# Optimization experiments

Measured on AMD Instinct MI355X. Metric: run time of the kernel, lower is better.

The kernel has to match this reference:

```python
import jax, jax.numpy as jnp
import numpy as np

N = 50000      # nodes
E = 800000     # edges
IN = 128       # in_channels
H = 128        # hidden_channels
C = 40         # num_classes
L = 2          # num_layers
BN_EPS = 1e-5


def setup_inputs() -> dict:
    key = jax.random.key(0)
    ks = jax.random.split(key, 16)
    s = 0.02
    return {
        "x": jax.random.normal(ks[0], (N, IN), dtype=jnp.float32),
        "edge_index": jax.random.randint(ks[1], (2, E), 0, N, dtype=jnp.int64),
        "fc0_w": jax.random.normal(ks[2], (H, IN), dtype=jnp.float32) * s,
        "fc0_b": jnp.zeros((H,), dtype=jnp.float32),
        "conv_w": jax.random.normal(ks[3], (L, H, H), dtype=jnp.float32) * s,
        "W_w": jax.random.normal(ks[4], (H, H), dtype=jnp.float32) * s,
        "W_b": jnp.zeros((H,), dtype=jnp.float32),
        "bn_gamma": jnp.ones((L + 1, H), dtype=jnp.float32),
        "bn_beta": jnp.zeros((L + 1, H), dtype=jnp.float32),
        "fc_out_w": jax.random.normal(ks[5], (H, H), dtype=jnp.float32) * s,
        "fc_out_b": jnp.zeros((H,), dtype=jnp.float32),
        "out_w": jax.random.normal(ks[6], (C, H), dtype=jnp.float32) * s,
        "out_b": jnp.zeros((C,), dtype=jnp.float32),
    }


def _bn_eval(x, gamma, beta):
    # eval-mode BatchNorm1d with default running stats (mean=0, var=1)
    return x * (gamma / jnp.sqrt(1.0 + BN_EPS)) + beta


def _gcn_conv(x, w, src, dst, norm, n):
    # x' = D^{-1/2} (A + I) D^{-1/2} (x @ w^T), bias=False
    xw = x @ w.T                        # [N, H]
    msg = xw[src] * norm[:, None]       # [E+N, H] gather + scale
    return jax.ops.segment_sum(msg, dst, num_segments=n)


def reference(x, edge_index, fc0_w, fc0_b, conv_w, W_w, W_b, bn_gamma, bn_beta,
              fc_out_w, fc_out_b, out_w, out_b):
    n = x.shape[0]
    loops = jnp.arange(n, dtype=edge_index.dtype)
    src = jnp.concatenate([edge_index[0], loops])   # add self-loops
    dst = jnp.concatenate([edge_index[1], loops])
    deg = jax.ops.segment_sum(jnp.ones_like(dst, dtype=x.dtype), dst, num_segments=n)
    deg_isqrt = jax.lax.rsqrt(deg)                  # deg >= 1 (self-loops)
    norm = deg_isqrt[src] * deg_isqrt[dst]          # [E+N]

    h = x @ fc0_w.T + fc0_b
    h = _bn_eval(h, bn_gamma[0], bn_beta[0])
    h = jax.nn.relu(h)                              # dropout: eval mode -> identity

    jk = h
    for i in range(L):
        h = _gcn_conv(h, conv_w[i], src, dst, norm, n)
        h = h @ W_w.T + W_b
        h = _bn_eval(h, bn_gamma[i + 1], bn_beta[i + 1])
        h = jax.nn.relu(h)
        jk = jnp.maximum(jk, h)                     # JumpingKnowledge 'max'

    out = jk @ fc_out_w.T + fc_out_b
    return out @ out_w.T + out_b
```

## Files before the change

kernel.cpp:

```cpp
#include <hip/hip_runtime.h>

#define NN 50000
#define NE 800000
#define EN 850000
#define NB 196
#define BINBLK 391
#define CAPE 5120
#define CAPT 5376

static constexpr float BN_SC = 0.99999500003749968f;

typedef __bf16 bf16x8 __attribute__((ext_vector_type(8)));
typedef float  f32x4  __attribute__((ext_vector_type(4)));

__device__ __forceinline__ float4 ld4(const float* p){ return *reinterpret_cast<const float4*>(p); }

__device__ __forceinline__ unsigned short f2bf(float f){
  union { float f; unsigned int i; } v; v.f = f;
  unsigned int r = v.i + 0x7fffu + ((v.i >> 16) & 1u);
  return (unsigned short)(r >> 16);
}
__device__ __forceinline__ float lo2f(unsigned int u){
  union { unsigned int i; float f; } v; v.i = u << 16; return v.f;
}
__device__ __forceinline__ float hi2f(unsigned int u){
  union { unsigned int i; float f; } v; v.i = u & 0xffff0000u; return v.f;
}
__device__ __forceinline__ unsigned int pk2(float flo, float fhi){
  return (unsigned int)f2bf(flo) | ((unsigned int)f2bf(fhi) << 16);
}
__device__ __forceinline__ int fragidx(int n, int k){
  int nt = n >> 4, c = n & 15, ks = k >> 5, g = (k >> 3) & 3, j = k & 7;
  return ((nt*4 + ks)*64 + g*16 + c)*8 + j;
}

extern "C" __global__ __launch_bounds__(256)
void k_prep(const float* __restrict__ fc0_w,
            const float* __restrict__ Ww, const float* __restrict__ cw,
            const float* __restrict__ ow, const float* __restrict__ fw,
            const float* __restrict__ fb, const float* __restrict__ ob,
            const int* __restrict__ ei,
            unsigned short* __restrict__ W0f, unsigned short* __restrict__ WC0f,
            unsigned short* __restrict__ WC1f, unsigned short* __restrict__ Wff,
            float* __restrict__ bfv, int* __restrict__ hists, int* __restrict__ gcur){
  int b = blockIdx.x;
  int t = threadIdx.x;
  if (b < 64){
    int idx = b*256 + t;
    int f = idx >> 7, k = idx & 127;
    W0f[fragidx(f, k)] = f2bf(fc0_w[f*128 + k]);
  } else if (b < 192){
    int idx = (b & 63)*256 + t;
    int f = idx >> 7, k = idx & 127;
    const float* c = (b < 128) ? cw : (cw + 16384);
    float acc = 0.f;
    #pragma unroll 4
    for (int j = 0; j < 128; ++j) acc = fmaf(Ww[f*128 + j], c[j*128 + k], acc);
    unsigned short* o = (b < 128) ? WC0f : WC1f;
    o[fragidx(f, k)] = f2bf(acc);
  } else if (b < 216){
    int idx = (b - 192)*256 + t;
    int c = idx >> 7, k = idx & 127;
    float acc = 0.f;
    if (c < 40){
      for (int j = 0; j < 128; ++j) acc = fmaf(ow[c*128 + j], fw[j*128 + k], acc);
    }
    Wff[fragidx(c, k)] = f2bf(acc);
    if (idx < 48){
      float a2 = 0.f;
      if (idx < 40){
        a2 = ob[idx];
        for (int j = 0; j < 128; ++j) a2 = fmaf(ow[idx*128 + j], fb[j], a2);
      }
      bfv[idx] = a2;
    }
  } else {
    __shared__ int h[NB];
    int bb = b - 216;
    if (t < NB) h[t] = 0;
    if (bb == 0 && t < NB) gcur[t] = t*CAPE;
    __syncthreads();
    int e0 = bb*2048;
    for (int i = t; i < 2048; i += 256){
      int e = e0 + i;
      if (e < NE) atomicAdd(&h[ei[NE+e] >> 8], 1);
    }
    __syncthreads();
    if (t < NB) hists[bb*NB + t] = h[t];
  }
}

extern "C" __global__ __launch_bounds__(256)
void k_bin(const int* __restrict__ ei, const int* __restrict__ hists,
           int* __restrict__ gcur, unsigned int* __restrict__ bbuf){
  __shared__ int lbase[NB], gbase[NB], hcur[NB];
  __shared__ int tot;
  __shared__ unsigned int stage[2048];
  __shared__ unsigned char bid[2048];
  int t = threadIdx.x;
  int bb = blockIdx.x;
  int h = (t < NB) ? hists[bb*NB + t] : 0;
  if (t < NB) lbase[t] = h;
  __syncthreads();
  if (t == 0){
    int run = 0;
    for (int b = 0; b < NB; ++b){ int x = lbase[b]; lbase[b] = run; run += x; }
    tot = run;
  }
  __syncthreads();
  if (t < NB && h > 0) gbase[t] = atomicAdd(&gcur[t], h);
  if (t < NB) hcur[t] = lbase[t];
  __syncthreads();
  int e0 = bb*2048;
  for (int i = t; i < 2048; i += 256){
    int e = e0 + i;
    if (e < NE){
      int s = ei[e], d = ei[NE+e];
      int b = d >> 8;
      int p = atomicAdd(&hcur[b], 1);
      stage[p] = ((unsigned int)d << 16) | (unsigned int)s;
      bid[p] = (unsigned char)b;
    }
  }
  __syncthreads();
  int m = tot;
  for (int j = t; j < m; j += 256){
    int b = bid[j];
    bbuf[gbase[b] + (j - lbase[b])] = stage[j];
  }
}

extern "C" __global__ __launch_bounds__(256)
void k_csr(const unsigned int* __restrict__ bbuf, const int* __restrict__ gcur,
           unsigned short* __restrict__ csr, int* __restrict__ offs,
           int* __restrict__ deg, float* __restrict__ dis){
  __shared__ int h[256], loff[256], lcur[256];
  __shared__ unsigned short stage[CAPT];
  int t = threadIdx.x;
  int b = blockIdx.x;
  int nb0 = b << 8;
  int BNv = min(256, NN - nb0);
  int ebeg = b*CAPE;
  int m = gcur[b] - ebeg;
  int base = b*CAPT;
  h[t] = (t < BNv) ? 1 : 0;
  __syncthreads();
  for (int i = t; i < m; i += 256)
    atomicAdd(&h[(bbuf[ebeg + i] >> 16) & 255], 1);
  __syncthreads();
  if (t == 0){
    int run = 0;
    for (int n = 0; n < BNv; ++n){ loff[n] = run; run += h[n]; }
  }
  __syncthreads();
  if (t < BNv){
    offs[nb0 + t] = base + loff[t];
    deg[nb0 + t] = h[t];
    dis[nb0 + t] = rsqrtf((float)h[t]);
    lcur[t] = loff[t] + 1;
    stage[loff[t]] = (unsigned short)(nb0 + t);
  }
  __syncthreads();
  for (int i = t; i < m; i += 256){
    unsigned int e = bbuf[ebeg + i];
    int p = atomicAdd(&lcur[(e >> 16) & 255], 1);
    stage[p] = (unsigned short)(e & 0xffffu);
  }
  __syncthreads();
  int M = m + BNv;
  for (int j = t; j < M; j += 256) csr[base + j] = stage[j];
}

extern "C" __global__ __launch_bounds__(256)
void k_gather(const unsigned short* __restrict__ Hf, const unsigned short* __restrict__ csr,
              const float* __restrict__ dis, const int* __restrict__ offs,
              const int* __restrict__ deg, unsigned short* __restrict__ Agg){
  int lane = threadIdx.x & 63;
  int node = blockIdx.x*4 + (threadIdx.x >> 6);
  int grp  = lane >> 4;
  int q8   = (lane & 15)*8;
  int start = offs[node];
  int n = deg[node];
  float dn = rsqrtf((float)n);
  float a0=0,a1=0,a2=0,a3=0,a4=0,a5=0,a6=0,a7=0;
  int nm1 = n - 1;
  for (int i = 0; i < n; i += 32){
    int s[8]; float w[8];
    #pragma unroll
    for (int j = 0; j < 8; ++j){
      int k = i + j*4 + grp;
      int c = min(k, nm1);
      s[j] = csr[start + c];
      w[j] = (k < n) ? dis[s[j]] : 0.f;
    }
    uint4 u[8];
    #pragma unroll
    for (int j = 0; j < 8; ++j)
      u[j] = *reinterpret_cast<const uint4*>(Hf + (size_t)s[j]*128 + q8);
    #pragma unroll
    for (int j = 0; j < 8; ++j){
      a0 = fmaf(lo2f(u[j].x), w[j], a0); a1 = fmaf(hi2f(u[j].x), w[j], a1);
      a2 = fmaf(lo2f(u[j].y), w[j], a2); a3 = fmaf(hi2f(u[j].y), w[j], a3);
      a4 = fmaf(lo2f(u[j].z), w[j], a4); a5 = fmaf(hi2f(u[j].z), w[j], a5);
      a6 = fmaf(lo2f(u[j].w), w[j], a6); a7 = fmaf(hi2f(u[j].w), w[j], a7);
    }
  }
  a0 += __shfl_xor(a0, 16); a1 += __shfl_xor(a1, 16);
  a2 += __shfl_xor(a2, 16); a3 += __shfl_xor(a3, 16);
  a4 += __shfl_xor(a4, 16); a5 += __shfl_xor(a5, 16);
  a6 += __shfl_xor(a6, 16); a7 += __shfl_xor(a7, 16);
  a0 += __shfl_xor(a0, 32); a1 += __shfl_xor(a1, 32);
  a2 += __shfl_xor(a2, 32); a3 += __shfl_xor(a3, 32);
  a4 += __shfl_xor(a4, 32); a5 += __shfl_xor(a5, 32);
  a6 += __shfl_xor(a6, 32); a7 += __shfl_xor(a7, 32);
  if (grp == 0){
    uint4 o;
    o.x = pk2(a0*dn, a1*dn);
    o.y = pk2(a2*dn, a3*dn);
    o.z = pk2(a4*dn, a5*dn);
    o.w = pk2(a6*dn, a7*dn);
    *reinterpret_cast<uint4*>(Agg + node*128 + q8) = o;
  }
}

template<int MODE>
__global__ __launch_bounds__(256)
void k_mm(const float* __restrict__ Xf, const unsigned short* __restrict__ Xb,
          const unsigned short* __restrict__ Wf, const float* __restrict__ bias,
          const float* __restrict__ gamma, const float* __restrict__ beta,
          unsigned short* __restrict__ Cout){
  __shared__ uint4 Ws4[2048];
  unsigned short* Ws = (unsigned short*)Ws4;
  const int t = threadIdx.x;
  {
    const uint4* src = reinterpret_cast<const uint4*>(Wf);
    #pragma unroll
    for (int i = 0; i < 8; ++i) Ws4[i*256 + t] = src[i*256 + t];
  }
  const int lane = t & 63;
  const int wv = t >> 6;
  const int m0 = blockIdx.x*64 + wv*16;
  const int mrow = min(m0 + (lane & 15), NN-1);
  const int kg = (lane >> 4)*8;
  bf16x8 a[4];
  if constexpr (MODE == 1){
    const float* px = Xf + (size_t)mrow*128 + kg;
    #pragma unroll
    for (int ks = 0; ks < 4; ++ks){
      float4 f0 = ld4(px + ks*32);
      float4 f1 = ld4(px + ks*32 + 4);
      bf16x8 aa;
      aa[0]=(__bf16)f0.x; aa[1]=(__bf16)f0.y; aa[2]=(__bf16)f0.z; aa[3]=(__bf16)f0.w;
      aa[4]=(__bf16)f1.x; aa[5]=(__bf16)f1.y; aa[6]=(__bf16)f1.z; aa[7]=(__bf16)f1.w;
      a[ks] = aa;
    }
  } else {
    const unsigned short* px = Xb + (size_t)mrow*128 + kg;
    #pragma unroll
    for (int ks = 0; ks < 4; ++ks)
      a[ks] = *reinterpret_cast<const bf16x8*>(px + ks*32);
  }
  __syncthreads();
  f32x4 acc[8];
  #pragma unroll
  for (int nt = 0; nt < 8; ++nt) acc[nt] = (f32x4){0.f,0.f,0.f,0.f};
  #pragma unroll
  for (int ks = 0; ks < 4; ++ks){
    #pragma unroll
    for (int nt = 0; nt < 8; ++nt){
      bf16x8 bfr = *reinterpret_cast<const bf16x8*>(Ws + ((nt*4 + ks)*64 + lane)*8);
      acc[nt] = __builtin_amdgcn_mfma_f32_16x16x32_bf16(a[ks], bfr, acc[nt], 0, 0, 0);
    }
  }
  __syncthreads();
  const int cB = lane & 15;
  const int r0 = (lane >> 4)*4;
  unsigned short* eld = Ws + wv*2176;
  #pragma unroll
  for (int nt = 0; nt < 8; ++nt){
    int cb = nt*16 + cB;
    float bi = bias[cb];
    float g  = gamma[cb]*BN_SC;
    float be = beta[cb];
    #pragma unroll
    for (int r = 0; r < 4; ++r){
      float o = fmaxf(fmaf(acc[nt][r] + bi, g, be), 0.f);
      eld[(r0 + r)*136 + cb] = f2bf(o);
    }
  }
  __syncthreads();
  {
    int lrow = t >> 2, seg = t & 3;
    int grow = blockIdx.x*64 + lrow;
    if (grow < NN){
      const unsigned short* src = Ws + (lrow >> 4)*2176 + (lrow & 15)*136 + seg*32;
      uint4* dst = reinterpret_cast<uint4*>(Cout + (size_t)grow*128 + seg*32);
      #pragma unroll
      for (int j = 0; j < 4; ++j) dst[j] = *reinterpret_cast<const uint4*>(src + j*8);
    }
  }
}

__global__ __launch_bounds__(256)
void k_mmf(const unsigned short* __restrict__ Xb, const unsigned short* __restrict__ Wf,
           const float* __restrict__ bias, const float* __restrict__ gamma,
           const float* __restrict__ beta,
           const unsigned short* __restrict__ H0, const unsigned short* __restrict__ H1,
           const unsigned short* __restrict__ Wff, const float* __restrict__ bfv,
           float* __restrict__ Out){
  __shared__ uint4 Ws4[2048];
  unsigned short* Ws = (unsigned short*)Ws4;
  const int t = threadIdx.x;
  {
    const uint4* src = reinterpret_cast<const uint4*>(Wf);
    #pragma unroll
    for (int i = 0; i < 8; ++i) Ws4[i*256 + t] = src[i*256 + t];
  }
  const int lane = t & 63;
  const int wv = t >> 6;
  const int m0 = blockIdx.x*64 + wv*16;
  const int mrow = min(m0 + (lane & 15), NN-1);
  const int kg = (lane >> 4)*8;
  bf16x8 a[4];
  {
    const unsigned short* px = Xb + (size_t)mrow*128 + kg;
    #pragma unroll
    for (int ks = 0; ks < 4; ++ks)
      a[ks] = *reinterpret_cast<const bf16x8*>(px + ks*32);
  }
  __syncthreads();
  f32x4 acc[8];
  #pragma unroll
  for (int nt = 0; nt < 8; ++nt) acc[nt] = (f32x4){0.f,0.f,0.f,0.f};
  #pragma unroll
  for (int ks = 0; ks < 4; ++ks){
    #pragma unroll
    for (int nt = 0; nt < 8; ++nt){
      bf16x8 bfr = *reinterpret_cast<const bf16x8*>(Ws + ((nt*4 + ks)*64 + lane)*8);
      acc[nt] = __builtin_amdgcn_mfma_f32_16x16x32_bf16(a[ks], bfr, acc[nt], 0, 0, 0);
    }
  }
  __syncthreads();
  const int cB = lane & 15;
  const int r0 = (lane >> 4)*4;
  unsigned short* eld = Ws + wv*2176;
  #pragma unroll
  for (int nt = 0; nt < 8; ++nt){
    int cb = nt*16 + cB;
    float bi = bias[cb];
    float g  = gamma[cb]*BN_SC;
    float be = beta[cb];
    #pragma unroll
    for (int r = 0; r < 4; ++r){
      float o = fmaxf(fmaf(acc[nt][r] + bi, g, be), 0.f);
      eld[(r0 + r)*136 + cb] = f2bf(o);
    }
  }
  const size_t pb = (size_t)mrow*128 + kg;
  const unsigned short* eldr = eld + (lane & 15)*136 + kg;
  bf16x8 af[4];
  #pragma unroll
  for (int ks = 0; ks < 4; ++ks){
    union U { uint4 v; unsigned short s[8]; } u0, u1, u2, r;
    u0.v = *reinterpret_cast<const uint4*>(H0 + pb + ks*32);
    u1.v = *reinterpret_cast<const uint4*>(H1 + pb + ks*32);
    u2.v = *reinterpret_cast<const uint4*>(eldr + ks*32);
    #pragma unroll
    for (int j = 0; j < 8; ++j){
      unsigned short m = u0.s[j] > u1.s[j] ? u0.s[j] : u1.s[j];
      r.s[j] = m > u2.s[j] ? m : u2.s[j];
    }
    af[ks] = *reinterpret_cast<bf16x8*>(&r);
  }
  f32x4 acc2[3];
  #pragma unroll
  for (int nt = 0; nt < 3; ++nt) acc2[nt] = (f32x4){0.f,0.f,0.f,0.f};
  #pragma unroll
  for (int ks = 0; ks < 4; ++ks){
    #pragma unroll
    for (int nt = 0; nt < 3; ++nt){
      bf16x8 bfr = *reinterpret_cast<const bf16x8*>(Wff + ((nt*4 + ks)*64 + lane)*8);
      acc2[nt] = __builtin_amdgcn_mfma_f32_16x16x32_bf16(af[ks], bfr, acc2[nt], 0, 0, 0);
    }
  }
  #pragma unroll
  for (int nt = 0; nt < 3; ++nt){
    int cb = nt*16 + cB;
    if (cb < 40){
      float bi = bfv[cb];
      #pragma unroll
      for (int r = 0; r < 4; ++r){
        int row = m0 + r0 + r;
        if (row < NN) Out[(size_t)row*40 + cb] = acc2[nt][r] + bi;
      }
    }
  }
}

extern "C" void kernel_launch(void* const* d_in, const int* in_sizes, int n_in,
                              void* d_out, int out_size, void* d_ws, size_t ws_size,
                              hipStream_t stream){
  const float* x     = (const float*)d_in[0];
  const int*   ei    = (const int*)d_in[1];
  const float* fc0_w = (const float*)d_in[2];
  const float* fc0_b = (const float*)d_in[3];
  const float* convw = (const float*)d_in[4];
  const float* Ww    = (const float*)d_in[5];
  const float* Wb    = (const float*)d_in[6];
  const float* bng   = (const float*)d_in[7];
  const float* bnb   = (const float*)d_in[8];
  const float* fow   = (const float*)d_in[9];
  const float* fob   = (const float*)d_in[10];
  const float* outw  = (const float*)d_in[11];
  const float* outb  = (const float*)d_in[12];
  float* out = (float*)d_out;

  char* p = (char*)d_ws;
  auto alloc = [&](size_t n){ char* r = p; p += (n + 255) & ~(size_t)255; return r; };
  int*   hists   = (int*)  alloc((size_t)BINBLK*NB*4);
  int*   gcur    = (int*)  alloc((size_t)NB*4);
  unsigned int*   bbuf  = (unsigned int*)  alloc((size_t)NB*CAPE*4);
  unsigned short* csr16 = (unsigned short*)alloc((size_t)NB*CAPT*2);
  int*   offs    = (int*)  alloc((size_t)NN*4);
  int*   deg     = (int*)  alloc((size_t)NN*4);
  float* dis     = (float*)alloc((size_t)NN*4);
  unsigned short* W0f  = (unsigned short*)alloc(16384*2);
  unsigned short* WC0f = (unsigned short*)alloc(16384*2);
  unsigned short* WC1f = (unsigned short*)alloc(16384*2);
  unsigned short* Wff  = (unsigned short*)alloc(6144*2);
  float* bfv     = (float*)alloc(64*4);
  unsigned short* H0  = (unsigned short*)alloc((size_t)NN*128*2);
  unsigned short* H1  = (unsigned short*)alloc((size_t)NN*128*2);
  unsigned short* AGG = (unsigned short*)alloc((size_t)NN*128*2);

  k_prep<<<216 + BINBLK, 256, 0, stream>>>(fc0_w, Ww, convw, outw, fow, fob, outb, ei,
                                           W0f, WC0f, WC1f, Wff, bfv, hists, gcur);
  k_bin<<<BINBLK, 256, 0, stream>>>(ei, hists, gcur, bbuf);
  k_csr<<<NB, 256, 0, stream>>>(bbuf, gcur, csr16, offs, deg, dis);

  k_mm<1><<<782, 256, 0, stream>>>(x, nullptr, W0f, fc0_b, bng, bnb, H0);
  k_gather<<<12500, 256, 0, stream>>>(H0, csr16, dis, offs, deg, AGG);
  k_mm<2><<<782, 256, 0, stream>>>(nullptr, AGG, WC0f, Wb, bng + 128, bnb + 128, H1);
  k_gather<<<12500, 256, 0, stream>>>(H1, csr16, dis, offs, deg, AGG);
  k_mmf<<<782, 256, 0, stream>>>(AGG, WC1f, Wb, bng + 256, bnb + 256,
                                 H0, H1, Wff, bfv, out);
}
```

Before: 151.7 us.

## Fuse edge binning with first GEMM in one launch and retile GEMM

The edge-binning pass and the first dense projection (x @ fc0_w) now run in one launch, with blocks split by index, so the two independent stages can overlap on the GPU and one kernel launch is removed. The matmul body is retiled to 32 rows per block, with each wave computing half of the output columns, which roughly doubles the block count. B fragments are now read directly from global memory instead of being staged in shared memory. The shared memory footprint shrinks, but each wave re-reads weight fragments from global or cache.

Result: faster. 146.0 us (-3.8%).

```diff
diff --git a/kernel.cpp b/kernel.cpp
--- a/kernel.cpp
+++ b/kernel.cpp
@@ -7,6 +7,7 @@
 #define BINBLK 391
 #define CAPE 5120
 #define CAPT 5376
+#define MMBLK 1563
 
 static constexpr float BN_SC = 0.99999500003749968f;
 
@@ -90,22 +91,22 @@
   }
 }
 
-extern "C" __global__ __launch_bounds__(256)
-void k_bin(const int* __restrict__ ei, const int* __restrict__ hists,
-           int* __restrict__ gcur, unsigned int* __restrict__ bbuf){
-  __shared__ int lbase[NB], gbase[NB], hcur[NB];
-  __shared__ int tot;
-  __shared__ unsigned int stage[2048];
-  __shared__ unsigned char bid[2048];
-  int t = threadIdx.x;
-  int bb = blockIdx.x;
+__device__ __forceinline__ void bin_body(int bb, int t, char* smem,
+    const int* __restrict__ ei, const int* __restrict__ hists,
+    int* __restrict__ gcur, unsigned int* __restrict__ bbuf){
+  int* lbase = (int*)smem;
+  int* gbase = lbase + NB;
+  int* hcur  = gbase + NB;
+  int* totp  = hcur + NB;
+  unsigned int* stage = (unsigned int*)(totp + 1);
+  unsigned char* bid = (unsigned char*)(stage + 2048);
   int h = (t < NB) ? hists[bb*NB + t] : 0;
   if (t < NB) lbase[t] = h;
   __syncthreads();
   if (t == 0){
     int run = 0;
     for (int b = 0; b < NB; ++b){ int x = lbase[b]; lbase[b] = run; run += x; }
-    tot = run;
+    *totp = run;
   }
   __syncthreads();
   if (t < NB && h > 0) gbase[t] = atomicAdd(&gcur[t], h);
@@ -123,11 +124,104 @@
     }
   }
   __syncthreads();
-  int m = tot;
+  int m = *totp;
   for (int j = t; j < m; j += 256){
     int b = bid[j];
     bbuf[gbase[b] + (j - lbase[b])] = stage[j];
   }
+}
+
+template<bool F32>
+__device__ __forceinline__ void mm_body(int blk, int t, char* smem,
+    const float* __restrict__ Xf, const unsigned short* __restrict__ Xb,
+    const unsigned short* __restrict__ Wf, const float* __restrict__ bias,
+    const float* __restrict__ gamma, const float* __restrict__ beta,
+    unsigned short* __restrict__ Cout){
+  unsigned short* eld = (unsigned short*)smem;
+  const int lane = t & 63;
+  const int wv = t >> 6;
+  const int pr = wv >> 1;
+  const int nh = wv & 1;
+  const int m0 = blk*32 + pr*16;
+  const int mrow = min(m0 + (lane & 15), NN-1);
+  const int kg = (lane >> 4)*8;
+  bf16x8 a[4];
+  if constexpr (F32){
+    const float* px = Xf + (size_t)mrow*128 + kg;
+    #pragma unroll
+    for (int ks = 0; ks < 4; ++ks){
+      float4 f0 = ld4(px + ks*32);
+      float4 f1 = ld4(px + ks*32 + 4);
+      bf16x8 aa;
+      aa[0]=(__bf16)f0.x; aa[1]=(__bf16)f0.y; aa[2]=(__bf16)f0.z; aa[3]=(__bf16)f0.w;
+      aa[4]=(__bf16)f1.x; aa[5]=(__bf16)f1.y; aa[6]=(__bf16)f1.z; aa[7]=(__bf16)f1.w;
+      a[ks] = aa;
+    }
+  } else {
+    const unsigned short* px = Xb + (size_t)mrow*128 + kg;
+    #pragma unroll
+    for (int ks = 0; ks < 4; ++ks)
+      a[ks] = *reinterpret_cast<const bf16x8*>(px + ks*32);
+  }
+  f32x4 acc[4];
+  #pragma unroll
+  for (int i = 0; i < 4; ++i) acc[i] = (f32x4){0.f,0.f,0.f,0.f};
+  #pragma unroll
+  for (int ks = 0; ks < 4; ++ks){
+    #pragma unroll
+    for (int ntl = 0; ntl < 4; ++ntl){
+      int nt = nh*4 + ntl;
+      bf16x8 bfr = *reinterpret_cast<const bf16x8*>(Wf + ((nt*4 + ks)*64 + lane)*8);
+      acc[ntl] = __builtin_amdgcn_mfma_f32_16x16x32_bf16(a[ks], bfr, acc[ntl], 0, 0, 0);
+    }
+  }
+  const int cB = lane & 15;
+  const int r0 = (lane >> 4)*4;
+  #pragma unroll
+  for (int ntl = 0; ntl < 4; ++ntl){
+    int cb = (nh*4 + ntl)*16 + cB;
+    float bi = bias[cb];
+    float g  = gamma[cb]*BN_SC;
+    float be = beta[cb];
+    #pragma unroll
+    for (int r = 0; r < 4; ++r){
+      float o = fmaxf(fmaf(acc[ntl][r] + bi, g, be), 0.f);
+      eld[(pr*16 + r0 + r)*136 + cb] = f2bf(o);
+    }
+  }
+  __syncthreads();
+  {
+    int row = t >> 3, seg = t & 7;
+    int grow = blk*32 + row;
+    if (grow < NN){
+      const unsigned short* src = eld + row*136 + seg*16;
+      uint4* dst = reinterpret_cast<uint4*>(Cout + (size_t)grow*128 + seg*16);
+      dst[0] = *reinterpret_cast<const uint4*>(src);
+      dst[1] = *reinterpret_cast<const uint4*>(src + 8);
+    }
+  }
+}
+
+extern "C" __global__ __launch_bounds__(256)
+void k_mix(const int* __restrict__ ei, const int* __restrict__ hists,
+           int* __restrict__ gcur, unsigned int* __restrict__ bbuf,
+           const float* __restrict__ x, const unsigned short* __restrict__ W0f,
+           const float* __restrict__ bias, const float* __restrict__ gamma,
+           const float* __restrict__ beta, unsigned short* __restrict__ H0){
+  __shared__ __align__(16) char smem[12608];
+  if (blockIdx.x < BINBLK)
+    bin_body(blockIdx.x, threadIdx.x, smem, ei, hists, gcur, bbuf);
+  else
+    mm_body<true>(blockIdx.x - BINBLK, threadIdx.x, smem, x, nullptr, W0f,
+                  bias, gamma, beta, H0);
+}
+
+extern "C" __global__ __launch_bounds__(256)
+void k_mm2(const unsigned short* __restrict__ Xb, const unsigned short* __restrict__ Wf,
+           const float* __restrict__ bias, const float* __restrict__ gamma,
+           const float* __restrict__ beta, unsigned short* __restrict__ Cout){
+  __shared__ __align__(16) char smem[8704];
+  mm_body<false>(blockIdx.x, threadIdx.x, smem, nullptr, Xb, Wf, bias, gamma, beta, Cout);
 }
 
 extern "C" __global__ __launch_bounds__(256)
@@ -150,7 +244,7 @@
   __syncthreads();
   if (t == 0){
     int run = 0;
-    for (int n = 0; n < BNv; ++n){ loff[n] = run; run += h[n]; }
+    for (int n = 0; n < BNv; ++n){ int x = h[n]; loff[n] = run; run += x; }
   }
   __syncthreads();
   if (t < BNv){
@@ -220,84 +314,6 @@
     o.z = pk2(a4*dn, a5*dn);
     o.w = pk2(a6*dn, a7*dn);
     *reinterpret_cast<uint4*>(Agg + node*128 + q8) = o;
-  }
-}
-
-template<int MODE>
-__global__ __launch_bounds__(256)
-void k_mm(const float* __restrict__ Xf, const unsigned short* __restrict__ Xb,
-          const unsigned short* __restrict__ Wf, const float* __restrict__ bias,
-          const float* __restrict__ gamma, const float* __restrict__ beta,
-          unsigned short* __restrict__ Cout){
-  __shared__ uint4 Ws4[2048];
-  unsigned short* Ws = (unsigned short*)Ws4;
-  const int t = threadIdx.x;
-  {
-    const uint4* src = reinterpret_cast<const uint4*>(Wf);
-    #pragma unroll
-    for (int i = 0; i < 8; ++i) Ws4[i*256 + t] = src[i*256 + t];
-  }
-  const int lane = t & 63;
-  const int wv = t >> 6;
-  const int m0 = blockIdx.x*64 + wv*16;
-  const int mrow = min(m0 + (lane & 15), NN-1);
-  const int kg = (lane >> 4)*8;
-  bf16x8 a[4];
-  if constexpr (MODE == 1){
-    const float* px = Xf + (size_t)mrow*128 + kg;
-    #pragma unroll
-    for (int ks = 0; ks < 4; ++ks){
-      float4 f0 = ld4(px + ks*32);
-      float4 f1 = ld4(px + ks*32 + 4);
-      bf16x8 aa;
-      aa[0]=(__bf16)f0.x; aa[1]=(__bf16)f0.y; aa[2]=(__bf16)f0.z; aa[3]=(__bf16)f0.w;
-      aa[4]=(__bf16)f1.x; aa[5]=(__bf16)f1.y; aa[6]=(__bf16)f1.z; aa[7]=(__bf16)f1.w;
-      a[ks] = aa;
-    }
-  } else {
-    const unsigned short* px = Xb + (size_t)mrow*128 + kg;
-    #pragma unroll
-    for (int ks = 0; ks < 4; ++ks)
-      a[ks] = *reinterpret_cast<const bf16x8*>(px + ks*32);
-  }
-  __syncthreads();
-  f32x4 acc[8];
-  #pragma unroll
-  for (int nt = 0; nt < 8; ++nt) acc[nt] = (f32x4){0.f,0.f,0.f,0.f};
-  #pragma unroll
-  for (int ks = 0; ks < 4; ++ks){
-    #pragma unroll
-    for (int nt = 0; nt < 8; ++nt){
-      bf16x8 bfr = *reinterpret_cast<const bf16x8*>(Ws + ((nt*4 + ks)*64 + lane)*8);
-      acc[nt] = __builtin_amdgcn_mfma_f32_16x16x32_bf16(a[ks], bfr, acc[nt], 0, 0, 0);
-    }
-  }
-  __syncthreads();
-  const int cB = lane & 15;
-  const int r0 = (lane >> 4)*4;
-  unsigned short* eld = Ws + wv*2176;
-  #pragma unroll
-  for (int nt = 0; nt < 8; ++nt){
-    int cb = nt*16 + cB;
-    float bi = bias[cb];
-    float g  = gamma[cb]*BN_SC;
-    float be = beta[cb];
-    #pragma unroll
-    for (int r = 0; r < 4; ++r){
-      float o = fmaxf(fmaf(acc[nt][r] + bi, g, be), 0.f);
-      eld[(r0 + r)*136 + cb] = f2bf(o);
-    }
-  }
-  __syncthreads();
-  {
-    int lrow = t >> 2, seg = t & 3;
-    int grow = blockIdx.x*64 + lrow;
-    if (grow < NN){
-      const unsigned short* src = Ws + (lrow >> 4)*2176 + (lrow & 15)*136 + seg*32;
-      uint4* dst = reinterpret_cast<uint4*>(Cout + (size_t)grow*128 + seg*32);
-      #pragma unroll
-      for (int j = 0; j < 4; ++j) dst[j] = *reinterpret_cast<const uint4*>(src + j*8);
-    }
   }
 }
 
@@ -435,12 +451,12 @@
 
   k_prep<<<216 + BINBLK, 256, 0, stream>>>(fc0_w, Ww, convw, outw, fow, fob, outb, ei,
                                            W0f, WC0f, WC1f, Wff, bfv, hists, gcur);
-  k_bin<<<BINBLK, 256, 0, stream>>>(ei, hists, gcur, bbuf);
+  k_mix<<<BINBLK + MMBLK, 256, 0, stream>>>(ei, hists, gcur, bbuf,
+                                            x, W0f, fc0_b, bng, bnb, H0);
   k_csr<<<NB, 256, 0, stream>>>(bbuf, gcur, csr16, offs, deg, dis);
 
-  k_mm<1><<<782, 256, 0, stream>>>(x, nullptr, W0f, fc0_b, bng, bnb, H0);
   k_gather<<<12500, 256, 0, stream>>>(H0, csr16, dis, offs, deg, AGG);
-  k_mm<2><<<782, 256, 0, stream>>>(nullptr, AGG, WC0f, Wb, bng + 128, bnb + 128, H1);
+  k_mm2<<<MMBLK, 256, 0, stream>>>(AGG, WC0f, Wb, bng + 128, bnb + 128, H1);
   k_gather<<<12500, 256, 0, stream>>>(H1, csr16, dis, offs, deg, AGG);
   k_mmf<<<782, 256, 0, stream>>>(AGG, WC1f, Wb, bng + 256, bnb + 256,
                                  H0, H1, Wff, bfv, out);
```
